# Kernel optimization log

Measured on AMD Instinct MI355X. Metric: run time of the kernel, lower is better.

## Reference

```python
import jax, jax.numpy as jnp
import numpy as np

# ---- module config (init_kwargs) ----
B, CIN, H, W_ = 2, 64, 56, 56
COUT, KH, KW = 128, 3, 3
K = CIN * KH * KW               # 576, reduction dim
ARRAY_ROWS = 128
IN_SLICES = (2, 2, 2, 2)        # 8-bit inputs, 2-bit slices
W_SLICES = (2, 2, 2, 2)         # 8-bit weights, 2-bit slices
N_STEPS_IN = 2 ** sum(IN_SLICES)    # 256, unsigned quantizer
N_STEPS_W = 2 ** sum(W_SLICES)      # 256
ADC_BINS = 256
ADC_STEP = 4.0

def _shifts_masks(slices):
    masks, shifts = [], [0]
    for s in slices[::-1]:
        masks.append((1 << s) - 1)
        shifts.append(s + shifts[-1])
    return np.array(shifts[-2::-1], np.int32), np.array(masks[::-1], np.int32)

_ish, _im = _shifts_masks(IN_SLICES)
_wsh, _wm = _shifts_masks(W_SLICES)
ISH, IM = jnp.asarray(_ish), jnp.asarray(_im)
WSH, WM = jnp.asarray(_wsh), jnp.asarray(_wm)
ISF = jnp.asarray((1 << _ish).astype(np.float32))  # slice recombine weights 2^shift
WSF = jnp.asarray((1 << _wsh).astype(np.float32))


def setup_inputs() -> dict:
    key = jax.random.key(0)
    k1, k2 = jax.random.split(key)
    return {
        "x": jax.random.normal(k1, (B, CIN, H, W_), jnp.float32),
        "w": jax.random.normal(k2, (COUT, CIN, KH, KW), jnp.float32),
    }


def _im2col(x):
    # 3x3 SAME conv patches, ordering [Cin, kh, kw] to match w.reshape(COUT, K)
    xp = jnp.pad(x, ((0, 0), (0, 0), (1, 1), (1, 1)))
    cols = jnp.stack([xp[:, :, i:i + H, j:j + W_]
                      for i in range(KH) for j in range(KW)], axis=2)  # [B,Cin,9,H,W]
    return cols.transpose(0, 3, 4, 1, 2).reshape(B * H * W_, K)  # [Nx, K]


def _quant_unsigned(v, n_steps):
    # Quantizer.offset + Quantizer.forward (unsigned, per-row over dim=-1)
    offs = v.min(axis=-1, keepdims=True)
    vr = v - offs
    step = vr.max(axis=-1, keepdims=True) / (n_steps - 1)
    q = jnp.round(jnp.clip(vr, 0.0, step * n_steps) / step).astype(jnp.int32)
    return q, step[..., 0], offs[..., 0]


def _slice_bits(q, shifts, masks):
    # Slicer.forward: stack (q >> shift) & mask along new leading slice dim
    s = shifts.reshape((-1,) + (1,) * q.ndim)
    m = masks.reshape((-1,) + (1,) * q.ndim)
    return (q[None] >> s) & m


def _chunk(t):
    # Chunker.forward over last dim K
    nb = -(-K // ARRAY_ROWS)
    npb = -(-K // nb)
    pad = nb * npb - K
    t = jnp.pad(t, [(0, 0)] * (t.ndim - 1) + [(0, pad)])
    t = t.reshape(t.shape[:-1] + (nb, npb))
    return jnp.moveaxis(t, -2, 0)  # [nb, ..., npb]


def reference(x, w):
    xf = _im2col(x)                    # [Nx, K]
    wf = w.reshape(COUT, K)            # [Ny, K]
    x_sum = xf.sum(axis=-1)            # [Nx]
    w_sum = wf.sum(axis=-1)            # [Ny]

    xq, x_scale, x_offs = _quant_unsigned(xf, N_STEPS_IN)
    wq, w_scale, w_offs = _quant_unsigned(wf, N_STEPS_W)

    xc = _chunk(_slice_bits(xq, ISH, IM))  # [nb, nis, Nx, npb] int32
    wc = _chunk(_slice_bits(wq, WSH, WM))  # [nb, nws, Ny, npb] int32

    # bit-serial crossbar MACs per (chunk, weight-slice, input-slice)
    z = jnp.einsum('bixk,bwyk->bwixy',
                   xc.astype(jnp.float32), wc.astype(jnp.float32))  # [nb,nws,nis,Nx,Ny]

    # ADC digitization (unsigned, fixed step): quantize then dequantize
    z = jnp.round(jnp.clip(z, 0.0, ADC_STEP * ADC_BINS) / ADC_STEP) * ADC_STEP

    # Chunker.reverse: sum crossbar blocks; Slicer.reverse: shift-weighted sums
    z = z.sum(axis=0)                               # [nws,nis,Nx,Ny]
    z = jnp.einsum('wixy,w,i->xy', z, WSF, ISF)     # [Nx,Ny]

    # dequantize scales and unsigned-offset correction:
    # x.y = sx*sy*(xq.yq) + x_offs*sum(y) + y_offs*sum(x) - x_offs*y_offs*K
    z = z * x_scale[:, None] * w_scale[None, :]
    z = (z + x_offs[:, None] * w_sum[None, :]
           + w_offs[None, :] * x_sum[:, None]
           - x_offs[:, None] * w_offs[None, :] * K)

    return z.reshape(B, H, W_, COUT).transpose(0, 3, 1, 2)  # [B,Cout,H,W]
```

## Files before the change

kernel.cpp:

```cpp
#include <hip/hip_runtime.h>


#define NXROW 6272
#define KDIM  576
#define NPB   116
#define SSTR  656

typedef int i32x4 __attribute__((ext_vector_type(4)));
typedef float f32x4 __attribute__((ext_vector_type(4)));

__device__ __forceinline__ i32x4 slice2b(i32x4 v, int sh) {
    i32x4 r;
    r[0] = (int)(((unsigned)v[0] >> sh) & 0x03030303u);
    r[1] = (int)(((unsigned)v[1] >> sh) & 0x03030303u);
    r[2] = (int)(((unsigned)v[2] >> sh) & 0x03030303u);
    r[3] = (int)(((unsigned)v[3] >> sh) & 0x03030303u);
    return r;
}

__global__ __launch_bounds__(256) void k_q(
    const float* __restrict__ x, const float* __restrict__ w,
    unsigned char* __restrict__ Xq, unsigned char* __restrict__ Wq,
    float* __restrict__ xsc, float* __restrict__ xof, float* __restrict__ xsm,
    float* __restrict__ wsc, float* __restrict__ wof, float* __restrict__ wsm)
{
    __shared__ __align__(16) unsigned char scr[4][SSTR];

    int tid = threadIdx.x, wv = tid >> 6, lane = tid & 63;
    int W = blockIdx.x * 4 + wv;
    unsigned char* myrow = scr[wv];

    if (lane < 16) {
        int col = lane < 12 ? (lane / 3) * 128 + 116 + (lane % 3) * 4
                            : 624 + (lane - 12) * 4;
        *(unsigned int*)(myrow + col) = 0u;
    }

    float v[9];
    unsigned char* dstbase;
    int rl;
    float *sc, *of, *sm;
    int sidx;

    if (W < NXROW) {
        int b = W >= 3136 ? 1 : 0;
        int pos = W - b * 3136;
        int hg = pos / 56, wg = pos - hg * 56;
        const float* xb = x + (size_t)(b * 64) * 3136;
#pragma unroll
        for (int r = 0; r < 9; r++) {
            int k = r * 64 + lane;
            int cin = k / 9;
            int off = k - cin * 9;
            int kh = off / 3;
            int kw = off - kh * 3;
            int hr = hg - 1 + kh, wc = wg - 1 + kw;
            bool ok = ((unsigned)hr < 56u) && ((unsigned)wc < 56u);
            v[r] = ok ? xb[cin * 3136 + hr * 56 + wc] : 0.f;
        }
        dstbase = Xq + (size_t)(W >> 4) * 10240;  rl = W & 15;
        sc = xsc; of = xof; sm = xsm; sidx = W;
    } else {
        int row = W - NXROW;
        const float* wr = w + (size_t)row * KDIM;
#pragma unroll
        for (int r = 0; r < 9; r++) v[r] = wr[r * 64 + lane];
        dstbase = Wq + (size_t)(row >> 4) * 10240;  rl = row & 15;
        sc = wsc; of = wof; sm = wsm; sidx = row;
    }

    float mn = v[0], mx = v[0], s = 0.f;
#pragma unroll
    for (int r = 0; r < 9; r++) { mn = fminf(mn, v[r]); mx = fmaxf(mx, v[r]); s += v[r]; }
#pragma unroll
    for (int off2 = 1; off2 < 64; off2 <<= 1) {
        mn = fminf(mn, __shfl_xor(mn, off2));
        mx = fmaxf(mx, __shfl_xor(mx, off2));
        s += __shfl_xor(s, off2);
    }
    float step = (mx - mn) / 255.0f;
    if (lane == 0) { sc[sidx] = step; of[sidx] = mn; sm[sidx] = s; }

#pragma unroll
    for (int r = 0; r < 9; r++) {
        int q = (int)rintf((v[r] - mn) / step);
        q = q < 0 ? 0 : (q > 255 ? 255 : q);
        int k = r * 64 + lane;
        int ch = k / NPB;
        myrow[k + 12 * ch] = (unsigned char)q;
    }
    __syncthreads();

    if (lane < 40) {
        int u = lane;
        i32x4 seg = *(const i32x4*)(myrow + u * 16);
        int dst16 = (u >> 3) * 128 + ((u >> 2) & 1) * 64 + (u & 3) * 16 + rl;
        *(i32x4*)(dstbase + (size_t)dst16 * 16) = seg;
    }
}

__device__ __forceinline__ void chunk_ws(const unsigned char* xt, const unsigned char* wt,
                                         int ch, int lane, i32x4 (&acc4)[4])
{
    const i32x4 zero = {0, 0, 0, 0};
    i32x4 x0 = *(const i32x4*)(xt + ch * 2048 + lane * 16);
    i32x4 x1 = *(const i32x4*)(xt + ch * 2048 + 1024 + lane * 16);
    i32x4 w0 = *(const i32x4*)(wt + ch * 2048 + lane * 16);
    i32x4 w1 = *(const i32x4*)(wt + ch * 2048 + 1024 + lane * 16);
    i32x4 ws0[4], ws1[4];
#pragma unroll
    for (int ws = 0; ws < 4; ws++) {
        ws0[ws] = slice2b(w0, 6 - 2 * ws);
        ws1[ws] = slice2b(w1, 6 - 2 * ws);
    }
#pragma unroll
    for (int is = 0; is < 4; is++) {
        int ish = 6 - 2 * is;
        i32x4 a0 = slice2b(x0, ish), a1 = slice2b(x1, ish);
#pragma unroll
        for (int ws = 0; ws < 4; ws++) {
            i32x4 d = __builtin_amdgcn_mfma_i32_16x16x64_i8(ws0[ws], a0, zero, 0, 0, 0);
            d = __builtin_amdgcn_mfma_i32_16x16x64_i8(ws1[ws], a1, d, 0, 0, 0);
            int sh = ish + 6 - 2 * ws;
#pragma unroll
            for (int r = 0; r < 4; r++) {
                int z = d[r];
                z = z > 1024 ? 1024 : z;
                int t = (z >> 2) & 1;
                int r4 = (z + 1 + t) & ~3;
                acc4[ws][r] += r4 << sh;
            }
        }
    }
}

__global__ __launch_bounds__(256) void k_d(
    const unsigned char* __restrict__ Xq, const unsigned char* __restrict__ Wq,
    const float* __restrict__ xscg, const float* __restrict__ xofg,
    const float* __restrict__ xsmg,
    const float* __restrict__ wscg, const float* __restrict__ wofg,
    const float* __restrict__ wsmg, float* __restrict__ out)
{
    __shared__ __align__(16) int pacc[2][64][4];

    int tid = threadIdx.x, wv = tid >> 6, lane = tid & 63;
    int g = lane >> 4, i16 = lane & 15;
    int blk = blockIdx.x;
    int ct = blk & 7, rp = blk >> 3;
    int tl = wv & 1, khalf = wv >> 1;
    int rtile = rp * 2 + tl;
    const unsigned char* xt = Xq + (size_t)rtile * 10240;
    const unsigned char* wt = Wq + (size_t)ct * 10240;

    i32x4 acc4[4] = {{0,0,0,0},{0,0,0,0},{0,0,0,0},{0,0,0,0}};
    if (khalf == 0) {
        chunk_ws(xt, wt, 0, lane, acc4);
        chunk_ws(xt, wt, 1, lane, acc4);
        chunk_ws(xt, wt, 2, lane, acc4);
    } else {
        chunk_ws(xt, wt, 3, lane, acc4);
        chunk_ws(xt, wt, 4, lane, acc4);
    }
    i32x4 acc;
#pragma unroll
    for (int r = 0; r < 4; r++)
        acc[r] = (acc4[0][r] + acc4[1][r]) + (acc4[2][r] + acc4[3][r]);

    if (khalf == 0) *(i32x4*)&pacc[tl][lane][0] = acc;
    __syncthreads();

    if (khalf == 1) {
        i32x4 p = *(const i32x4*)&pacc[tl][lane][0];
#pragma unroll
        for (int r = 0; r < 4; r++) acc[r] += p[r];

        int b = rtile >= 196 ? 1 : 0;
        int xrow = rtile * 16 + i16;
        float xs_ = xscg[xrow], xo = xofg[xrow], xsv = xsmg[xrow];
        int hw = (rtile - 196 * b) * 16 + i16;
#pragma unroll
        for (int r = 0; r < 4; r++) {
            int wrow = ct * 16 + g * 4 + r;
            float tt = ((float)acc[r] * xs_) * wscg[wrow];
            float res = ((tt + xo * wsmg[wrow]) + wofg[wrow] * xsv)
                      - (xo * wofg[wrow]) * 576.0f;
            out[(size_t)(b * 128 + wrow) * 3136 + hw] = res;
        }
    }
}

extern "C" void kernel_launch(void* const* d_in, const int* in_sizes, int n_in,
                              void* d_out, int out_size, void* d_ws, size_t ws_size,
                              hipStream_t stream) {
    const float* x = (const float*)d_in[0];
    const float* w = (const float*)d_in[1];
    float* out = (float*)d_out;

    unsigned char* Xq = (unsigned char*)d_ws;
    unsigned char* Wq = Xq + (size_t)392 * 10240;
    float* xsc = (float*)(Wq + 8 * 10240);
    float* xof = xsc + NXROW;
    float* xsm = xof + NXROW;
    float* wsc = xsm + NXROW;
    float* wof = wsc + 128;
    float* wsm = wof + 128;

    hipLaunchKernelGGL(k_q, dim3(1600), dim3(256), 0, stream,
                       x, w, Xq, Wq, xsc, xof, xsm, wsc, wof, wsm);
    hipLaunchKernelGGL(k_d, dim3(1568), dim3(256), 0, stream,
                       Xq, Wq, xsc, xof, xsm, wsc, wof, wsm, out);
}
```

Before: 33.90 us.

## Fuse input quantization into the MFMA kernel via LDS, keep separate weight quant

Input im2col gathering and per-row quantization now happen inside the main MFMA kernel and are written straight to shared memory. The global Xq buffer and its per-row scale, offset and sum arrays are gone, which removes a global write and read round trip and part of the launch dependency. Only the small weight quantization stays in its own kernel. In exchange, each 16-row tile is now quantized redundantly by the 4 blocks that cover different output-channel quarters, so the gather and reduction work on x is repeated four times.

```diff
diff --git a/kernel.cpp b/kernel.cpp
--- a/kernel.cpp
+++ b/kernel.cpp
@@ -7,7 +7,6 @@
 #define SSTR  656
 
 typedef int i32x4 __attribute__((ext_vector_type(4)));
-typedef float f32x4 __attribute__((ext_vector_type(4)));
 
 __device__ __forceinline__ i32x4 slice2b(i32x4 v, int sh) {
     i32x4 r;
@@ -18,35 +17,119 @@
     return r;
 }
 
-__global__ __launch_bounds__(256) void k_q(
-    const float* __restrict__ x, const float* __restrict__ w,
-    unsigned char* __restrict__ Xq, unsigned char* __restrict__ Wq,
-    float* __restrict__ xsc, float* __restrict__ xof, float* __restrict__ xsm,
-    float* __restrict__ wsc, float* __restrict__ wof, float* __restrict__ wsm)
-{
-    __shared__ __align__(16) unsigned char scr[4][SSTR];
-
-    int tid = threadIdx.x, wv = tid >> 6, lane = tid & 63;
-    int W = blockIdx.x * 4 + wv;
-    unsigned char* myrow = scr[wv];
-
+__device__ __forceinline__ void rowquant_to_lds(const float (&v)[9],
+                                                unsigned char* myrow, int lane,
+                                                float* scp, float* ofp, float* smp)
+{
     if (lane < 16) {
         int col = lane < 12 ? (lane / 3) * 128 + 116 + (lane % 3) * 4
                             : 624 + (lane - 12) * 4;
         *(unsigned int*)(myrow + col) = 0u;
     }
-
+    float mn = v[0], mx = v[0], s = 0.f;
+#pragma unroll
+    for (int r = 0; r < 9; r++) { mn = fminf(mn, v[r]); mx = fmaxf(mx, v[r]); s += v[r]; }
+#pragma unroll
+    for (int off2 = 1; off2 < 64; off2 <<= 1) {
+        mn = fminf(mn, __shfl_xor(mn, off2));
+        mx = fmaxf(mx, __shfl_xor(mx, off2));
+        s += __shfl_xor(s, off2);
+    }
+    float step = (mx - mn) / 255.0f;
+    if (lane == 0) { *scp = step; *ofp = mn; *smp = s; }
+#pragma unroll
+    for (int r = 0; r < 9; r++) {
+        int q = (int)rintf((v[r] - mn) / step);
+        q = q < 0 ? 0 : (q > 255 ? 255 : q);
+        int k = r * 64 + lane;
+        int ch = k / NPB;
+        myrow[k + 12 * ch] = (unsigned char)q;
+    }
+}
+
+__global__ __launch_bounds__(256) void k_wq(
+    const float* __restrict__ w, unsigned char* __restrict__ Wq,
+    float* __restrict__ wsc, float* __restrict__ wof, float* __restrict__ wsm)
+{
+    __shared__ __align__(16) unsigned char scr[4][SSTR];
+    int tid = threadIdx.x, wv = tid >> 6, lane = tid & 63;
+    int row = blockIdx.x * 4 + wv;
+    unsigned char* myrow = scr[wv];
+
+    const float* wr = w + (size_t)row * KDIM;
     float v[9];
-    unsigned char* dstbase;
-    int rl;
-    float *sc, *of, *sm;
-    int sidx;
-
-    if (W < NXROW) {
-        int b = W >= 3136 ? 1 : 0;
-        int pos = W - b * 3136;
+#pragma unroll
+    for (int r = 0; r < 9; r++) v[r] = wr[r * 64 + lane];
+
+    rowquant_to_lds(v, myrow, lane, wsc + row, wof + row, wsm + row);
+    __syncthreads();
+
+    if (lane < 40) {
+        int u = lane;
+        i32x4 seg = *(const i32x4*)(myrow + u * 16);
+        int dst16 = (u >> 3) * 128 + ((u >> 2) & 1) * 64 + (u & 3) * 16 + (row & 15);
+        *(i32x4*)(Wq + (size_t)(row >> 4) * 10240 + (size_t)dst16 * 16) = seg;
+    }
+}
+
+__device__ __forceinline__ void chunk_ws(const unsigned char* xp, const unsigned char* wt,
+                                         int ch, int lane, i32x4 (&acc4)[4])
+{
+    const i32x4 zero = {0, 0, 0, 0};
+    i32x4 x0 = *(const i32x4*)(xp + ch * 128);
+    i32x4 x1 = *(const i32x4*)(xp + ch * 128 + 64);
+    i32x4 w0 = *(const i32x4*)(wt + ch * 2048 + lane * 16);
+    i32x4 w1 = *(const i32x4*)(wt + ch * 2048 + 1024 + lane * 16);
+    i32x4 ws0[4], ws1[4];
+#pragma unroll
+    for (int ws = 0; ws < 4; ws++) {
+        ws0[ws] = slice2b(w0, 6 - 2 * ws);
+        ws1[ws] = slice2b(w1, 6 - 2 * ws);
+    }
+#pragma unroll
+    for (int is = 0; is < 4; is++) {
+        int ish = 6 - 2 * is;
+        i32x4 a0 = slice2b(x0, ish), a1 = slice2b(x1, ish);
+#pragma unroll
+        for (int ws = 0; ws < 4; ws++) {
+            i32x4 d = __builtin_amdgcn_mfma_i32_16x16x64_i8(ws0[ws], a0, zero, 0, 0, 0);
+            d = __builtin_amdgcn_mfma_i32_16x16x64_i8(ws1[ws], a1, d, 0, 0, 0);
+            int sh = ish + 6 - 2 * ws;
+#pragma unroll
+            for (int r = 0; r < 4; r++) {
+                int z = d[r];
+                z = z > 1024 ? 1024 : z;
+                int t = (z >> 2) & 1;
+                int r4 = (z + 1 + t) & ~3;
+                acc4[ws][r] += r4 << sh;
+            }
+        }
+    }
+}
+
+__global__ __launch_bounds__(256) void k_main(
+    const float* __restrict__ x, const unsigned char* __restrict__ Wq,
+    const float* __restrict__ wscg, const float* __restrict__ wofg,
+    const float* __restrict__ wsmg, float* __restrict__ out)
+{
+    __shared__ __align__(16) unsigned char scrX[16 * SSTR];
+    __shared__ __align__(16) int pacc[2][64][4];
+    __shared__ float xscl[16], xofl[16], xsml[16];
+
+    int tid = threadIdx.x, wv = tid >> 6, lane = tid & 63;
+    int g = lane >> 4, i16 = lane & 15;
+    int blk = blockIdx.x;
+    int rtile = blk >> 2, cq = blk & 3;
+    int b = rtile >= 196 ? 1 : 0;
+    int pos0 = (rtile - 196 * b) * 16;
+    const float* xb = x + (size_t)(b * 64) * 3136;
+
+#pragma unroll
+    for (int q = 0; q < 4; q++) {
+        int i = wv * 4 + q;
+        int pos = pos0 + i;
         int hg = pos / 56, wg = pos - hg * 56;
-        const float* xb = x + (size_t)(b * 64) * 3136;
+        float v[9];
 #pragma unroll
         for (int r = 0; r < 9; r++) {
             int k = r * 64 + lane;
@@ -58,126 +141,39 @@
             bool ok = ((unsigned)hr < 56u) && ((unsigned)wc < 56u);
             v[r] = ok ? xb[cin * 3136 + hr * 56 + wc] : 0.f;
         }
-        dstbase = Xq + (size_t)(W >> 4) * 10240;  rl = W & 15;
-        sc = xsc; of = xof; sm = xsm; sidx = W;
-    } else {
-        int row = W - NXROW;
-        const float* wr = w + (size_t)row * KDIM;
-#pragma unroll
-        for (int r = 0; r < 9; r++) v[r] = wr[r * 64 + lane];
-        dstbase = Wq + (size_t)(row >> 4) * 10240;  rl = row & 15;
-        sc = wsc; of = wof; sm = wsm; sidx = row;
-    }
-
-    float mn = v[0], mx = v[0], s = 0.f;
-#pragma unroll
-    for (int r = 0; r < 9; r++) { mn = fminf(mn, v[r]); mx = fmaxf(mx, v[r]); s += v[r]; }
-#pragma unroll
-    for (int off2 = 1; off2 < 64; off2 <<= 1) {
-        mn = fminf(mn, __shfl_xor(mn, off2));
-        mx = fmaxf(mx, __shfl_xor(mx, off2));
-        s += __shfl_xor(s, off2);
-    }
-    float step = (mx - mn) / 255.0f;
-    if (lane == 0) { sc[sidx] = step; of[sidx] = mn; sm[sidx] = s; }
-
-#pragma unroll
-    for (int r = 0; r < 9; r++) {
-        int q = (int)rintf((v[r] - mn) / step);
-        q = q < 0 ? 0 : (q > 255 ? 255 : q);
-        int k = r * 64 + lane;
-        int ch = k / NPB;
-        myrow[k + 12 * ch] = (unsigned char)q;
+        rowquant_to_lds(v, scrX + i * SSTR, lane, xscl + i, xofl + i, xsml + i);
     }
     __syncthreads();
 
-    if (lane < 40) {
-        int u = lane;
-        i32x4 seg = *(const i32x4*)(myrow + u * 16);
-        int dst16 = (u >> 3) * 128 + ((u >> 2) & 1) * 64 + (u & 3) * 16 + rl;
-        *(i32x4*)(dstbase + (size_t)dst16 * 16) = seg;
-    }
-}
-
-__device__ __forceinline__ void chunk_ws(const unsigned char* xt, const unsigned char* wt,
-                                         int ch, int lane, i32x4 (&acc4)[4])
-{
-    const i32x4 zero = {0, 0, 0, 0};
-    i32x4 x0 = *(const i32x4*)(xt + ch * 2048 + lane * 16);
-    i32x4 x1 = *(const i32x4*)(xt + ch * 2048 + 1024 + lane * 16);
-    i32x4 w0 = *(const i32x4*)(wt + ch * 2048 + lane * 16);
-    i32x4 w1 = *(const i32x4*)(wt + ch * 2048 + 1024 + lane * 16);
-    i32x4 ws0[4], ws1[4];
-#pragma unroll
-    for (int ws = 0; ws < 4; ws++) {
-        ws0[ws] = slice2b(w0, 6 - 2 * ws);
-        ws1[ws] = slice2b(w1, 6 - 2 * ws);
-    }
-#pragma unroll
-    for (int is = 0; is < 4; is++) {
-        int ish = 6 - 2 * is;
-        i32x4 a0 = slice2b(x0, ish), a1 = slice2b(x1, ish);
-#pragma unroll
-        for (int ws = 0; ws < 4; ws++) {
-            i32x4 d = __builtin_amdgcn_mfma_i32_16x16x64_i8(ws0[ws], a0, zero, 0, 0, 0);
-            d = __builtin_amdgcn_mfma_i32_16x16x64_i8(ws1[ws], a1, d, 0, 0, 0);
-            int sh = ish + 6 - 2 * ws;
-#pragma unroll
-            for (int r = 0; r < 4; r++) {
-                int z = d[r];
-                z = z > 1024 ? 1024 : z;
-                int t = (z >> 2) & 1;
-                int r4 = (z + 1 + t) & ~3;
-                acc4[ws][r] += r4 << sh;
-            }
-        }
-    }
-}
-
-__global__ __launch_bounds__(256) void k_d(
-    const unsigned char* __restrict__ Xq, const unsigned char* __restrict__ Wq,
-    const float* __restrict__ xscg, const float* __restrict__ xofg,
-    const float* __restrict__ xsmg,
-    const float* __restrict__ wscg, const float* __restrict__ wofg,
-    const float* __restrict__ wsmg, float* __restrict__ out)
-{
-    __shared__ __align__(16) int pacc[2][64][4];
-
-    int tid = threadIdx.x, wv = tid >> 6, lane = tid & 63;
-    int g = lane >> 4, i16 = lane & 15;
-    int blk = blockIdx.x;
-    int ct = blk & 7, rp = blk >> 3;
-    int tl = wv & 1, khalf = wv >> 1;
-    int rtile = rp * 2 + tl;
-    const unsigned char* xt = Xq + (size_t)rtile * 10240;
+    int ctl_l = wv & 1, khalf = wv >> 1;
+    int ct = cq * 2 + ctl_l;
+    const unsigned char* xp = scrX + i16 * SSTR + g * 16;
     const unsigned char* wt = Wq + (size_t)ct * 10240;
 
     i32x4 acc4[4] = {{0,0,0,0},{0,0,0,0},{0,0,0,0},{0,0,0,0}};
     if (khalf == 0) {
-        chunk_ws(xt, wt, 0, lane, acc4);
-        chunk_ws(xt, wt, 1, lane, acc4);
-        chunk_ws(xt, wt, 2, lane, acc4);
+        chunk_ws(xp, wt, 0, lane, acc4);
+        chunk_ws(xp, wt, 1, lane, acc4);
+        chunk_ws(xp, wt, 2, lane, acc4);
     } else {
-        chunk_ws(xt, wt, 3, lane, acc4);
-        chunk_ws(xt, wt, 4, lane, acc4);
+        chunk_ws(xp, wt, 3, lane, acc4);
+        chunk_ws(xp, wt, 4, lane, acc4);
     }
     i32x4 acc;
 #pragma unroll
     for (int r = 0; r < 4; r++)
         acc[r] = (acc4[0][r] + acc4[1][r]) + (acc4[2][r] + acc4[3][r]);
 
-    if (khalf == 0) *(i32x4*)&pacc[tl][lane][0] = acc;
+    if (khalf == 0) *(i32x4*)&pacc[ctl_l][lane][0] = acc;
     __syncthreads();
 
     if (khalf == 1) {
-        i32x4 p = *(const i32x4*)&pacc[tl][lane][0];
+        i32x4 p = *(const i32x4*)&pacc[ctl_l][lane][0];
 #pragma unroll
         for (int r = 0; r < 4; r++) acc[r] += p[r];
 
-        int b = rtile >= 196 ? 1 : 0;
-        int xrow = rtile * 16 + i16;
-        float xs_ = xscg[xrow], xo = xofg[xrow], xsv = xsmg[xrow];
-        int hw = (rtile - 196 * b) * 16 + i16;
+        float xs_ = xscl[i16], xo = xofl[i16], xsv = xsml[i16];
+        int hw = pos0 + i16;
 #pragma unroll
         for (int r = 0; r < 4; r++) {
             int wrow = ct * 16 + g * 4 + r;
@@ -196,17 +192,13 @@
     const float* w = (const float*)d_in[1];
     float* out = (float*)d_out;
 
-    unsigned char* Xq = (unsigned char*)d_ws;
-    unsigned char* Wq = Xq + (size_t)392 * 10240;
-    float* xsc = (float*)(Wq + 8 * 10240);
-    float* xof = xsc + NXROW;
-    float* xsm = xof + NXROW;
-    float* wsc = xsm + NXROW;
+    unsigned char* Wq = (unsigned char*)d_ws;
+    float* wsc = (float*)(Wq + 8 * 10240);
     float* wof = wsc + 128;
     float* wsm = wof + 128;
 
-    hipLaunchKernelGGL(k_q, dim3(1600), dim3(256), 0, stream,
-                       x, w, Xq, Wq, xsc, xof, xsm, wsc, wof, wsm);
-    hipLaunchKernelGGL(k_d, dim3(1568), dim3(256), 0, stream,
-                       Xq, Wq, xsc, xof, xsm, wsc, wof, wsm, out);
-}
+    hipLaunchKernelGGL(k_wq, dim3(32), dim3(256), 0, stream,
+                       w, Wq, wsc, wof, wsm);
+    hipLaunchKernelGGL(k_main, dim3(1568), dim3(256), 0, stream,
+                       x, Wq, wsc, wof, wsm, out);
+}
```

Measured after the change: 46.96 us. 38.5% more time.

## Split input slices across waves and batch 16-row tiles in quantize kernel

Applied to the files above, without the earlier changes.

The quantize kernel now uses 1024-thread blocks that each handle a full 16-row tile. It transposes the tile through LDS and writes it out as one contiguous store, instead of each wave writing scattered 16-byte segments. The dot kernel now gives each block a single 16x16 output tile and stages the X tile into LDS. Each wave handles one input bit-slice across all five chunks, and the four partial sums are reduced through shared memory. This doubles the grid and spreads the MFMA work more evenly, at the cost of an extra LDS staging pass and a sync.

```diff
diff --git a/kernel.cpp b/kernel.cpp
--- a/kernel.cpp
+++ b/kernel.cpp
@@ -7,7 +7,6 @@
 #define SSTR  656
 
 typedef int i32x4 __attribute__((ext_vector_type(4)));
-typedef float f32x4 __attribute__((ext_vector_type(4)));
 
 __device__ __forceinline__ i32x4 slice2b(i32x4 v, int sh) {
     i32x4 r;
@@ -18,33 +17,52 @@
     return r;
 }
 
-__global__ __launch_bounds__(256) void k_q(
+__device__ __forceinline__ void rowquant_to_lds(const float (&v)[9],
+                                                unsigned char* myrow, int lane,
+                                                float* scp, float* ofp, float* smp)
+{
+    if (lane < 16) {
+        int col = lane < 12 ? (lane / 3) * 128 + 116 + (lane % 3) * 4
+                            : 624 + (lane - 12) * 4;
+        *(unsigned int*)(myrow + col) = 0u;
+    }
+    float mn = v[0], mx = v[0], s = 0.f;
+#pragma unroll
+    for (int r = 0; r < 9; r++) { mn = fminf(mn, v[r]); mx = fmaxf(mx, v[r]); s += v[r]; }
+#pragma unroll
+    for (int off2 = 1; off2 < 64; off2 <<= 1) {
+        mn = fminf(mn, __shfl_xor(mn, off2));
+        mx = fmaxf(mx, __shfl_xor(mx, off2));
+        s += __shfl_xor(s, off2);
+    }
+    float step = (mx - mn) / 255.0f;
+    if (lane == 0) { *scp = step; *ofp = mn; *smp = s; }
+#pragma unroll
+    for (int r = 0; r < 9; r++) {
+        int q = (int)rintf((v[r] - mn) / step);
+        q = q < 0 ? 0 : (q > 255 ? 255 : q);
+        int k = r * 64 + lane;
+        int ch = k / NPB;
+        myrow[k + 12 * ch] = (unsigned char)q;
+    }
+}
+
+__global__ __launch_bounds__(1024) void k_q(
     const float* __restrict__ x, const float* __restrict__ w,
     unsigned char* __restrict__ Xq, unsigned char* __restrict__ Wq,
     float* __restrict__ xsc, float* __restrict__ xof, float* __restrict__ xsm,
     float* __restrict__ wsc, float* __restrict__ wof, float* __restrict__ wsm)
 {
-    __shared__ __align__(16) unsigned char scr[4][SSTR];
+    __shared__ __align__(16) unsigned char scrT[16][SSTR];
 
     int tid = threadIdx.x, wv = tid >> 6, lane = tid & 63;
-    int W = blockIdx.x * 4 + wv;
-    unsigned char* myrow = scr[wv];
-
-    if (lane < 16) {
-        int col = lane < 12 ? (lane / 3) * 128 + 116 + (lane % 3) * 4
-                            : 624 + (lane - 12) * 4;
-        *(unsigned int*)(myrow + col) = 0u;
-    }
+    int blk = blockIdx.x;
 
     float v[9];
-    unsigned char* dstbase;
-    int rl;
-    float *sc, *of, *sm;
-    int sidx;
-
-    if (W < NXROW) {
-        int b = W >= 3136 ? 1 : 0;
-        int pos = W - b * 3136;
+    if (blk < 392) {
+        int R = blk * 16 + wv;
+        int b = R >= 3136 ? 1 : 0;
+        int pos = R - b * 3136;
         int hg = pos / 56, wg = pos - hg * 56;
         const float* xb = x + (size_t)(b * 64) * 3136;
 #pragma unroll
@@ -58,69 +76,63 @@
             bool ok = ((unsigned)hr < 56u) && ((unsigned)wc < 56u);
             v[r] = ok ? xb[cin * 3136 + hr * 56 + wc] : 0.f;
         }
-        dstbase = Xq + (size_t)(W >> 4) * 10240;  rl = W & 15;
-        sc = xsc; of = xof; sm = xsm; sidx = W;
+        rowquant_to_lds(v, scrT[wv], lane, xsc + R, xof + R, xsm + R);
     } else {
-        int row = W - NXROW;
+        int row = (blk - 392) * 16 + wv;
         const float* wr = w + (size_t)row * KDIM;
 #pragma unroll
         for (int r = 0; r < 9; r++) v[r] = wr[r * 64 + lane];
-        dstbase = Wq + (size_t)(row >> 4) * 10240;  rl = row & 15;
-        sc = wsc; of = wof; sm = wsm; sidx = row;
-    }
-
-    float mn = v[0], mx = v[0], s = 0.f;
-#pragma unroll
-    for (int r = 0; r < 9; r++) { mn = fminf(mn, v[r]); mx = fmaxf(mx, v[r]); s += v[r]; }
-#pragma unroll
-    for (int off2 = 1; off2 < 64; off2 <<= 1) {
-        mn = fminf(mn, __shfl_xor(mn, off2));
-        mx = fmaxf(mx, __shfl_xor(mx, off2));
-        s += __shfl_xor(s, off2);
-    }
-    float step = (mx - mn) / 255.0f;
-    if (lane == 0) { sc[sidx] = step; of[sidx] = mn; sm[sidx] = s; }
-
-#pragma unroll
-    for (int r = 0; r < 9; r++) {
-        int q = (int)rintf((v[r] - mn) / step);
-        q = q < 0 ? 0 : (q > 255 ? 255 : q);
-        int k = r * 64 + lane;
-        int ch = k / NPB;
-        myrow[k + 12 * ch] = (unsigned char)q;
+        rowquant_to_lds(v, scrT[wv], lane, wsc + row, wof + row, wsm + row);
     }
     __syncthreads();
 
-    if (lane < 40) {
-        int u = lane;
-        i32x4 seg = *(const i32x4*)(myrow + u * 16);
-        int dst16 = (u >> 3) * 128 + ((u >> 2) & 1) * 64 + (u & 3) * 16 + rl;
-        *(i32x4*)(dstbase + (size_t)dst16 * 16) = seg;
+    unsigned char* dst = blk < 392 ? Xq + (size_t)blk * 10240
+                                   : Wq + (size_t)(blk - 392) * 10240;
+    if (tid < 640) {
+        int rl = tid & 15;
+        int u = (tid >> 7) * 8 + ((tid >> 6) & 1) * 4 + ((tid >> 4) & 3);
+        *(i32x4*)(dst + (size_t)tid * 16) = *(const i32x4*)(&scrT[rl][u * 16]);
     }
 }
 
-__device__ __forceinline__ void chunk_ws(const unsigned char* xt, const unsigned char* wt,
-                                         int ch, int lane, i32x4 (&acc4)[4])
+__global__ __launch_bounds__(256) void k_d(
+    const unsigned char* __restrict__ Xq, const unsigned char* __restrict__ Wq,
+    const float* __restrict__ xscg, const float* __restrict__ xofg,
+    const float* __restrict__ xsmg,
+    const float* __restrict__ wscg, const float* __restrict__ wofg,
+    const float* __restrict__ wsmg, float* __restrict__ out)
 {
+    __shared__ __align__(16) unsigned char xlds[10240];
+    __shared__ __align__(16) int pacc[4][64][4];
+
+    int tid = threadIdx.x, wv = tid >> 6, lane = tid & 63;
+    int g = lane >> 4, i16 = lane & 15;
+    int blk = blockIdx.x;
+    int ct = blk & 7, rtile = blk >> 3;
+    const unsigned char* xt = Xq + (size_t)rtile * 10240;
+    const unsigned char* wt = Wq + (size_t)ct * 10240;
+
+    for (int idx = tid; idx < 640; idx += 256)
+        *(i32x4*)(xlds + (size_t)idx * 16) = *(const i32x4*)(xt + (size_t)idx * 16);
+    __syncthreads();
+
+    int ish = 6 - 2 * wv;
     const i32x4 zero = {0, 0, 0, 0};
-    i32x4 x0 = *(const i32x4*)(xt + ch * 2048 + lane * 16);
-    i32x4 x1 = *(const i32x4*)(xt + ch * 2048 + 1024 + lane * 16);
-    i32x4 w0 = *(const i32x4*)(wt + ch * 2048 + lane * 16);
-    i32x4 w1 = *(const i32x4*)(wt + ch * 2048 + 1024 + lane * 16);
-    i32x4 ws0[4], ws1[4];
+    i32x4 acc4[4] = {{0,0,0,0},{0,0,0,0},{0,0,0,0},{0,0,0,0}};
+
 #pragma unroll
-    for (int ws = 0; ws < 4; ws++) {
-        ws0[ws] = slice2b(w0, 6 - 2 * ws);
-        ws1[ws] = slice2b(w1, 6 - 2 * ws);
-    }
-#pragma unroll
-    for (int is = 0; is < 4; is++) {
-        int ish = 6 - 2 * is;
+    for (int ch = 0; ch < 5; ch++) {
+        i32x4 x0 = *(const i32x4*)(xlds + ch * 2048 + lane * 16);
+        i32x4 x1 = *(const i32x4*)(xlds + ch * 2048 + 1024 + lane * 16);
+        i32x4 w0 = *(const i32x4*)(wt + ch * 2048 + lane * 16);
+        i32x4 w1 = *(const i32x4*)(wt + ch * 2048 + 1024 + lane * 16);
         i32x4 a0 = slice2b(x0, ish), a1 = slice2b(x1, ish);
 #pragma unroll
         for (int ws = 0; ws < 4; ws++) {
-            i32x4 d = __builtin_amdgcn_mfma_i32_16x16x64_i8(ws0[ws], a0, zero, 0, 0, 0);
-            d = __builtin_amdgcn_mfma_i32_16x16x64_i8(ws1[ws], a1, d, 0, 0, 0);
+            i32x4 b0 = slice2b(w0, 6 - 2 * ws);
+            i32x4 b1 = slice2b(w1, 6 - 2 * ws);
+            i32x4 d = __builtin_amdgcn_mfma_i32_16x16x64_i8(b0, a0, zero, 0, 0, 0);
+            d = __builtin_amdgcn_mfma_i32_16x16x64_i8(b1, a1, d, 0, 0, 0);
             int sh = ish + 6 - 2 * ws;
 #pragma unroll
             for (int r = 0; r < 4; r++) {
@@ -132,47 +144,22 @@
             }
         }
     }
-}
 
-__global__ __launch_bounds__(256) void k_d(
-    const unsigned char* __restrict__ Xq, const unsigned char* __restrict__ Wq,
-    const float* __restrict__ xscg, const float* __restrict__ xofg,
-    const float* __restrict__ xsmg,
-    const float* __restrict__ wscg, const float* __restrict__ wofg,
-    const float* __restrict__ wsmg, float* __restrict__ out)
-{
-    __shared__ __align__(16) int pacc[2][64][4];
-
-    int tid = threadIdx.x, wv = tid >> 6, lane = tid & 63;
-    int g = lane >> 4, i16 = lane & 15;
-    int blk = blockIdx.x;
-    int ct = blk & 7, rp = blk >> 3;
-    int tl = wv & 1, khalf = wv >> 1;
-    int rtile = rp * 2 + tl;
-    const unsigned char* xt = Xq + (size_t)rtile * 10240;
-    const unsigned char* wt = Wq + (size_t)ct * 10240;
-
-    i32x4 acc4[4] = {{0,0,0,0},{0,0,0,0},{0,0,0,0},{0,0,0,0}};
-    if (khalf == 0) {
-        chunk_ws(xt, wt, 0, lane, acc4);
-        chunk_ws(xt, wt, 1, lane, acc4);
-        chunk_ws(xt, wt, 2, lane, acc4);
-    } else {
-        chunk_ws(xt, wt, 3, lane, acc4);
-        chunk_ws(xt, wt, 4, lane, acc4);
-    }
     i32x4 acc;
 #pragma unroll
     for (int r = 0; r < 4; r++)
         acc[r] = (acc4[0][r] + acc4[1][r]) + (acc4[2][r] + acc4[3][r]);
 
-    if (khalf == 0) *(i32x4*)&pacc[tl][lane][0] = acc;
+    if (wv != 0) *(i32x4*)&pacc[wv][lane][0] = acc;
     __syncthreads();
 
-    if (khalf == 1) {
-        i32x4 p = *(const i32x4*)&pacc[tl][lane][0];
+    if (wv == 0) {
+        i32x4 p1 = *(const i32x4*)&pacc[1][lane][0];
+        i32x4 p2 = *(const i32x4*)&pacc[2][lane][0];
+        i32x4 p3 = *(const i32x4*)&pacc[3][lane][0];
 #pragma unroll
-        for (int r = 0; r < 4; r++) acc[r] += p[r];
+        for (int r = 0; r < 4; r++)
+            acc[r] = (acc[r] + p1[r]) + (p2[r] + p3[r]);
 
         int b = rtile >= 196 ? 1 : 0;
         int xrow = rtile * 16 + i16;
@@ -205,8 +192,8 @@
     float* wof = wsc + 128;
     float* wsm = wof + 128;
 
-    hipLaunchKernelGGL(k_q, dim3(1600), dim3(256), 0, stream,
+    hipLaunchKernelGGL(k_q, dim3(400), dim3(1024), 0, stream,
                        x, w, Xq, Wq, xsc, xof, xsm, wsc, wof, wsm);
-    hipLaunchKernelGGL(k_d, dim3(1568), dim3(256), 0, stream,
+    hipLaunchKernelGGL(k_d, dim3(3136), dim3(256), 0, stream,
                        Xq, Wq, xsc, xof, xsm, wsc, wof, wsm, out);
 }
```

After: 36.33 us. 7.2% more time.

## Split MAC work across waves by input bit-slice instead of K-chunk halves

Applied to the files above, without the earlier changes.

The matmul kernel now gives each block a single 16x16 output tile. Each of its four waves handles one input bit-slice across all five K chunks, where before two waves split the chunks unevenly (three versus two) and each block covered two row tiles. Partial sums from the four waves are combined through shared memory by wave 0, which also applies the dequantize epilogue. This balances MFMA work across waves and doubles the grid size. The cost is that every wave reloads the same X and W tiles, which adds L2 traffic, and the epilogue is now serialized on one wave.

```diff
diff --git a/kernel.cpp b/kernel.cpp
--- a/kernel.cpp
+++ b/kernel.cpp
@@ -7,7 +7,6 @@
 #define SSTR  656
 
 typedef int i32x4 __attribute__((ext_vector_type(4)));
-typedef float f32x4 __attribute__((ext_vector_type(4)));
 
 __device__ __forceinline__ i32x4 slice2b(i32x4 v, int sh) {
     i32x4 r;
@@ -99,28 +98,39 @@
     }
 }
 
-__device__ __forceinline__ void chunk_ws(const unsigned char* xt, const unsigned char* wt,
-                                         int ch, int lane, i32x4 (&acc4)[4])
+__global__ __launch_bounds__(256) void k_d(
+    const unsigned char* __restrict__ Xq, const unsigned char* __restrict__ Wq,
+    const float* __restrict__ xscg, const float* __restrict__ xofg,
+    const float* __restrict__ xsmg,
+    const float* __restrict__ wscg, const float* __restrict__ wofg,
+    const float* __restrict__ wsmg, float* __restrict__ out)
 {
+    __shared__ __align__(16) int pacc[4][64][4];
+
+    int tid = threadIdx.x, wv = tid >> 6, lane = tid & 63;
+    int g = lane >> 4, i16 = lane & 15;
+    int blk = blockIdx.x;
+    int ct = blk & 7, rtile = blk >> 3;
+    const unsigned char* xt = Xq + (size_t)rtile * 10240 + lane * 16;
+    const unsigned char* wt = Wq + (size_t)ct * 10240 + lane * 16;
+
+    int ish = 6 - 2 * wv;
     const i32x4 zero = {0, 0, 0, 0};
-    i32x4 x0 = *(const i32x4*)(xt + ch * 2048 + lane * 16);
-    i32x4 x1 = *(const i32x4*)(xt + ch * 2048 + 1024 + lane * 16);
-    i32x4 w0 = *(const i32x4*)(wt + ch * 2048 + lane * 16);
-    i32x4 w1 = *(const i32x4*)(wt + ch * 2048 + 1024 + lane * 16);
-    i32x4 ws0[4], ws1[4];
+    i32x4 acc4[4] = {{0,0,0,0},{0,0,0,0},{0,0,0,0},{0,0,0,0}};
+
 #pragma unroll
-    for (int ws = 0; ws < 4; ws++) {
-        ws0[ws] = slice2b(w0, 6 - 2 * ws);
-        ws1[ws] = slice2b(w1, 6 - 2 * ws);
-    }
-#pragma unroll
-    for (int is = 0; is < 4; is++) {
-        int ish = 6 - 2 * is;
+    for (int ch = 0; ch < 5; ch++) {
+        i32x4 x0 = *(const i32x4*)(xt + ch * 2048);
+        i32x4 x1 = *(const i32x4*)(xt + ch * 2048 + 1024);
+        i32x4 w0 = *(const i32x4*)(wt + ch * 2048);
+        i32x4 w1 = *(const i32x4*)(wt + ch * 2048 + 1024);
         i32x4 a0 = slice2b(x0, ish), a1 = slice2b(x1, ish);
 #pragma unroll
         for (int ws = 0; ws < 4; ws++) {
-            i32x4 d = __builtin_amdgcn_mfma_i32_16x16x64_i8(ws0[ws], a0, zero, 0, 0, 0);
-            d = __builtin_amdgcn_mfma_i32_16x16x64_i8(ws1[ws], a1, d, 0, 0, 0);
+            i32x4 b0 = slice2b(w0, 6 - 2 * ws);
+            i32x4 b1 = slice2b(w1, 6 - 2 * ws);
+            i32x4 d = __builtin_amdgcn_mfma_i32_16x16x64_i8(b0, a0, zero, 0, 0, 0);
+            d = __builtin_amdgcn_mfma_i32_16x16x64_i8(b1, a1, d, 0, 0, 0);
             int sh = ish + 6 - 2 * ws;
 #pragma unroll
             for (int r = 0; r < 4; r++) {
@@ -132,47 +142,22 @@
             }
         }
     }
-}
 
-__global__ __launch_bounds__(256) void k_d(
-    const unsigned char* __restrict__ Xq, const unsigned char* __restrict__ Wq,
-    const float* __restrict__ xscg, const float* __restrict__ xofg,
-    const float* __restrict__ xsmg,
-    const float* __restrict__ wscg, const float* __restrict__ wofg,
-    const float* __restrict__ wsmg, float* __restrict__ out)
-{
-    __shared__ __align__(16) int pacc[2][64][4];
-
-    int tid = threadIdx.x, wv = tid >> 6, lane = tid & 63;
-    int g = lane >> 4, i16 = lane & 15;
-    int blk = blockIdx.x;
-    int ct = blk & 7, rp = blk >> 3;
-    int tl = wv & 1, khalf = wv >> 1;
-    int rtile = rp * 2 + tl;
-    const unsigned char* xt = Xq + (size_t)rtile * 10240;
-    const unsigned char* wt = Wq + (size_t)ct * 10240;
-
-    i32x4 acc4[4] = {{0,0,0,0},{0,0,0,0},{0,0,0,0},{0,0,0,0}};
-    if (khalf == 0) {
-        chunk_ws(xt, wt, 0, lane, acc4);
-        chunk_ws(xt, wt, 1, lane, acc4);
-        chunk_ws(xt, wt, 2, lane, acc4);
-    } else {
-        chunk_ws(xt, wt, 3, lane, acc4);
-        chunk_ws(xt, wt, 4, lane, acc4);
-    }
     i32x4 acc;
 #pragma unroll
     for (int r = 0; r < 4; r++)
         acc[r] = (acc4[0][r] + acc4[1][r]) + (acc4[2][r] + acc4[3][r]);
 
-    if (khalf == 0) *(i32x4*)&pacc[tl][lane][0] = acc;
+    if (wv != 0) *(i32x4*)&pacc[wv][lane][0] = acc;
     __syncthreads();
 
-    if (khalf == 1) {
-        i32x4 p = *(const i32x4*)&pacc[tl][lane][0];
+    if (wv == 0) {
+        i32x4 p1 = *(const i32x4*)&pacc[1][lane][0];
+        i32x4 p2 = *(const i32x4*)&pacc[2][lane][0];
+        i32x4 p3 = *(const i32x4*)&pacc[3][lane][0];
 #pragma unroll
-        for (int r = 0; r < 4; r++) acc[r] += p[r];
+        for (int r = 0; r < 4; r++)
+            acc[r] = (acc[r] + p1[r]) + (p2[r] + p3[r]);
 
         int b = rtile >= 196 ? 1 : 0;
         int xrow = rtile * 16 + i16;
@@ -207,6 +192,6 @@
 
     hipLaunchKernelGGL(k_q, dim3(1600), dim3(256), 0, stream,
                        x, w, Xq, Wq, xsc, xof, xsm, wsc, wof, wsm);
-    hipLaunchKernelGGL(k_d, dim3(1568), dim3(256), 0, stream,
+    hipLaunchKernelGGL(k_d, dim3(3136), dim3(256), 0, stream,
                        Xq, Wq, xsc, xof, xsm, wsc, wof, wsm, out);
 }
```

After: 34.06 us. Within noise of the previous version (+0.5%).
